# Kernel optimization log

Hardware: AMD Instinct MI355X
Metric: run time of the kernel (lower is better)

Reference implementation:

```python
import jax, jax.numpy as jnp
import numpy as np

E = 1024
H = 16
D = E // H  # head_dim = 64
B = 4
S = 2048


def setup_inputs() -> dict:
    key = jax.random.key(0)
    ks = jax.random.split(key, 10)
    sc = 1.0 / np.sqrt(E)
    return {
        "inputs": jax.random.normal(ks[0], (B, S, E), dtype=jnp.float32),
        "wq": jax.random.normal(ks[1], (E, E), dtype=jnp.float32) * sc,
        "bq": jnp.zeros((E,), dtype=jnp.float32),
        "wk": jax.random.normal(ks[2], (E, E), dtype=jnp.float32) * sc,
        "bk": jnp.zeros((E,), dtype=jnp.float32),
        "wv": jax.random.normal(ks[3], (E, E), dtype=jnp.float32) * sc,
        "bv": jnp.zeros((E,), dtype=jnp.float32),
        "wo": jax.random.normal(ks[4], (E, E), dtype=jnp.float32) * sc,
        "bo": jnp.zeros((E,), dtype=jnp.float32),
        "ln_gamma": jnp.ones((E,), dtype=jnp.float32),
        "ln_beta": jnp.zeros((E,), dtype=jnp.float32),
    }


def reference(inputs, wq, bq, wk, bk, wv, bv, wo, bo, ln_gamma, ln_beta):
    # QKV projections, split heads: [B,S,E] -> [B,H,S,D]
    def split_heads(x):
        return x.reshape(B, S, H, D).transpose(0, 2, 1, 3)

    q = split_heads(inputs @ wq + bq)
    k = split_heads(inputs @ wk + bk)
    v = split_heads(inputs @ wv + bv)

    scale = 1.0 / jnp.sqrt(jnp.asarray(D, dtype=inputs.dtype))
    score = jnp.einsum("bhqd,bhkd->bhqk", q, k) * scale  # [B,H,S,S]
    weights = jax.nn.softmax(score, axis=-1)
    out = jnp.einsum("bhqk,bhkd->bhqd", weights, v)  # [B,H,S,D]
    out = out.transpose(0, 2, 1, 3).reshape(B, S, E)
    out = out @ wo + bo

    # residual + LayerNorm(eps=1e-6)
    x = inputs + out
    mean = jnp.mean(x, axis=-1, keepdims=True)
    var = jnp.mean(jnp.square(x - mean), axis=-1, keepdims=True)
    x = (x - mean) * jax.lax.rsqrt(var + 1e-6)
    return x * ln_gamma + ln_beta
```

## Files before the change

### kernel.cpp

```cpp
#include <hip/hip_runtime.h>

#define E_DIM 1024
#define H_NUM 16
#define D_DIM 64
#define B_NUM 4
#define S_DIM 2048
#define M_DIM 8192

#define SCALE_Q 0.18033688011112042f
#define SMAX 10.0f

typedef _Float16 f16;
typedef __attribute__((ext_vector_type(4))) _Float16 f16x4;
typedef __attribute__((ext_vector_type(8))) _Float16 f16x8;
typedef __attribute__((ext_vector_type(2))) __fp16 h16x2;
typedef __attribute__((ext_vector_type(4))) float f32x4;

extern "C" __device__ float __ocml_native_exp2_f32(float);

#define MFMA32(a, b, c) __builtin_amdgcn_mfma_f32_16x16x32_f16(a, b, c, 0, 0, 0)

#define GLOBAL_LOAD_LDS_16(gp, lp)                                    \
  __builtin_amdgcn_global_load_lds(                                   \
      (const __attribute__((address_space(1))) void*)(gp),            \
      (__attribute__((address_space(3))) void*)(lp), 16, 0, 0)

__global__ __launch_bounds__(256) void k_convert_x(const float* __restrict__ x,
                                                   f16* __restrict__ xh) {
  size_t i = ((size_t)blockIdx.x * 256 + threadIdx.x) * 4;
  float4 v = *reinterpret_cast<const float4*>(x + i);
  f16x4 o = {(f16)v.x, (f16)v.y, (f16)v.z, (f16)v.w};
  *reinterpret_cast<f16x4*>(xh + i) = o;
}

__global__ __launch_bounds__(256) void k_transpose_w(
    const float* __restrict__ w0, const float* __restrict__ w1,
    const float* __restrict__ w2, const float* __restrict__ w3,
    f16* __restrict__ dst) {
  __shared__ float tile[32][33];
  const float* src = blockIdx.z == 0 ? w0 : blockIdx.z == 1 ? w1
                   : blockIdx.z == 2 ? w2 : w3;
  f16* out = dst + (size_t)blockIdx.z * (E_DIM * E_DIM);
  const int n0 = blockIdx.x * 32, k0 = blockIdx.y * 32;
  const int tx = threadIdx.x & 31, ty = threadIdx.x >> 5;
#pragma unroll
  for (int i = 0; i < 4; i++)
    tile[ty + i * 8][tx] = src[(size_t)(k0 + ty + i * 8) * E_DIM + n0 + tx];
  __syncthreads();
#pragma unroll
  for (int i = 0; i < 4; i++)
    out[(size_t)(n0 + ty + i * 8) * E_DIM + k0 + tx] = (f16)tile[tx][ty + i * 8];
}

__global__ __launch_bounds__(256) void k_gemm_qkv(
    const f16* __restrict__ A, const f16* __restrict__ BT3,
    const float* __restrict__ bq, const float* __restrict__ bk,
    const float* __restrict__ bv, f16* __restrict__ Qb,
    f16* __restrict__ Kb, f16* __restrict__ VT) {
  __shared__ short As[2][128 * 64];
  __shared__ short Bs[2][128 * 64];
  const int m0 = blockIdx.y * 128, n0 = blockIdx.x * 128;
  const int region = blockIdx.x >> 3;
  const float* bias = region == 0 ? bq : region == 1 ? bk : bv;
  const float scale = region == 0 ? SCALE_Q : 1.0f;
  const int t = threadIdx.x;
  const int wave = t >> 6, lane = t & 63;
  const int l15 = lane & 15, quad = lane >> 4;
  const int wm = (wave & 1) * 64, wn = (wave >> 1) * 64;
  const int er0 = t >> 3;
  const int ecs = (((t & 7) ^ (er0 & 7))) * 8;
  const int el = (t & 7) * 8;

  const f16* gA[4];
  const f16* gB[4];
  int eo[4];
#pragma unroll
  for (int i = 0; i < 4; i++) {
    const int r = er0 + i * 32;
    gA[i] = A + (size_t)(m0 + r) * E_DIM + ecs;
    gB[i] = BT3 + (size_t)(n0 + r) * E_DIM + ecs;
    eo[i] = r * 64 + el;
  }
  auto issue = [&](int bf) {
#pragma unroll
    for (int i = 0; i < 4; i++) {
      GLOBAL_LOAD_LDS_16(gA[i], &As[bf][eo[i]]);
      GLOBAL_LOAD_LDS_16(gB[i], &Bs[bf][eo[i]]);
      gA[i] += 64;
      gB[i] += 64;
    }
  };

  issue(0);
  f32x4 acc[4][4] = {};

  for (int kt = 0; kt < E_DIM / 64; kt++) {
    __syncthreads();
    if (kt + 1 < E_DIM / 64) issue((kt + 1) & 1);
    const short* as = As[kt & 1];
    const short* bs = Bs[kt & 1];
#pragma unroll
    for (int ks = 0; ks < 2; ks++) {
      f16x8 af[4], bfr[4];
#pragma unroll
      for (int i = 0; i < 4; i++) {
        const int cg = ((ks * 4 + quad) ^ (l15 & 7)) * 8;
        af[i]  = *reinterpret_cast<const f16x8*>(&as[(wm + i * 16 + l15) * 64 + cg]);
        bfr[i] = *reinterpret_cast<const f16x8*>(&bs[(wn + i * 16 + l15) * 64 + cg]);
      }
#pragma unroll
      for (int mi = 0; mi < 4; mi++)
#pragma unroll
        for (int ni = 0; ni < 4; ni++)
          acc[mi][ni] = MFMA32(af[mi], bfr[ni], acc[mi][ni]);
    }
  }
#pragma unroll
  for (int ni = 0; ni < 4; ni++) {
    const int col = ((n0 + wn + ni * 16 + l15) & 1023);
    const float bv_ = bias[col];
    const int hh = col >> 6, dd = col & 63;
#pragma unroll
    for (int mi = 0; mi < 4; mi++) {
#pragma unroll
      for (int r = 0; r < 4; r++) {
        const int row = m0 + wm + mi * 16 + quad * 4 + r;
        const f16 v = (f16)((acc[mi][ni][r] + bv_) * scale);
        if (region == 0) {
          Qb[(size_t)row * E_DIM + col] = v;
        } else if (region == 1) {
          Kb[(size_t)row * E_DIM + col] = v;
        } else {
          const int bb = row >> 11, ss = row & 2047;
          VT[(((size_t)bb * H_NUM + hh) * D_DIM + dd) * S_DIM + ss] = v;
        }
      }
    }
  }
}

__global__ __launch_bounds__(256) void k_gemm(
    const f16* __restrict__ A, const f16* __restrict__ BT,
    const float* __restrict__ bias, f16* __restrict__ Cout) {
  __shared__ short As[2][128 * 64];
  __shared__ short Bs[2][128 * 64];
  const int m0 = blockIdx.y * 128, n0 = blockIdx.x * 128;
  const int t = threadIdx.x;
  const int wave = t >> 6, lane = t & 63;
  const int l15 = lane & 15, quad = lane >> 4;
  const int wm = (wave & 1) * 64, wn = (wave >> 1) * 64;
  const int er0 = t >> 3;
  const int ecs = (((t & 7) ^ (er0 & 7))) * 8;
  const int el = (t & 7) * 8;

  const f16* gA[4];
  const f16* gB[4];
  int eo[4];
#pragma unroll
  for (int i = 0; i < 4; i++) {
    const int r = er0 + i * 32;
    gA[i] = A + (size_t)(m0 + r) * E_DIM + ecs;
    gB[i] = BT + (size_t)(n0 + r) * E_DIM + ecs;
    eo[i] = r * 64 + el;
  }
  auto issue = [&](int bf) {
#pragma unroll
    for (int i = 0; i < 4; i++) {
      GLOBAL_LOAD_LDS_16(gA[i], &As[bf][eo[i]]);
      GLOBAL_LOAD_LDS_16(gB[i], &Bs[bf][eo[i]]);
      gA[i] += 64;
      gB[i] += 64;
    }
  };

  issue(0);
  f32x4 acc[4][4] = {};

  for (int kt = 0; kt < E_DIM / 64; kt++) {
    __syncthreads();
    if (kt + 1 < E_DIM / 64) issue((kt + 1) & 1);
    const short* as = As[kt & 1];
    const short* bs = Bs[kt & 1];
#pragma unroll
    for (int ks = 0; ks < 2; ks++) {
      f16x8 af[4], bfr[4];
#pragma unroll
      for (int i = 0; i < 4; i++) {
        const int cg = ((ks * 4 + quad) ^ (l15 & 7)) * 8;
        af[i]  = *reinterpret_cast<const f16x8*>(&as[(wm + i * 16 + l15) * 64 + cg]);
        bfr[i] = *reinterpret_cast<const f16x8*>(&bs[(wn + i * 16 + l15) * 64 + cg]);
      }
#pragma unroll
      for (int mi = 0; mi < 4; mi++)
#pragma unroll
        for (int ni = 0; ni < 4; ni++)
          acc[mi][ni] = MFMA32(af[mi], bfr[ni], acc[mi][ni]);
    }
  }
#pragma unroll
  for (int ni = 0; ni < 4; ni++) {
    const int col = n0 + wn + ni * 16 + l15;
    const float bv = bias[col];
#pragma unroll
    for (int mi = 0; mi < 4; mi++) {
#pragma unroll
      for (int r = 0; r < 4; r++) {
        const int row = m0 + wm + mi * 16 + quad * 4 + r;
        Cout[(size_t)row * E_DIM + col] = (f16)(acc[mi][ni][r] + bv);
      }
    }
  }
}

__global__ __launch_bounds__(256) void k_attention(
    const f16* __restrict__ Q, const f16* __restrict__ K,
    const f16* __restrict__ VT, f16* __restrict__ O) {
  __shared__ short Ks[2][64 * 64];
  __shared__ short Vs[2][64 * 64];
  const int bh = blockIdx.x, qt = blockIdx.y;
  const int b = bh >> 4, h = bh & 15;
  const int t = threadIdx.x;
  const int wave = t >> 6, lane = t & 63, l15 = lane & 15, quad = lane >> 4;
  const size_t rowbase = (size_t)b * S_DIM;
  const int ch = h * D_DIM;
  const int qb = qt * 128 + wave * 32;

  f16x8 qf[2][2];
#pragma unroll
  for (int g = 0; g < 2; g++) {
    const size_t qrow = rowbase + qb + g * 16 + l15;
    qf[g][0] = *reinterpret_cast<const f16x8*>(Q + qrow * E_DIM + ch + quad * 8);
    qf[g][1] = *reinterpret_cast<const f16x8*>(Q + qrow * E_DIM + ch + 32 + quad * 8);
  }

  f32x4 o_acc[2][4] = {};
  f32x4 l_acc[2] = {};
  const f16x8 ones8 = {(f16)1.f, (f16)1.f, (f16)1.f, (f16)1.f,
                       (f16)1.f, (f16)1.f, (f16)1.f, (f16)1.f};

  const int cgp = lane & 7;
  const f16* vtb = VT + ((size_t)(b * H_NUM + h) * D_DIM) * S_DIM;
  const f16* kgp[2];
  const f16* vgp[2];
  int ofs[2];
#pragma unroll
  for (int i = 0; i < 2; i++) {
    const int slot = wave * 16 + i * 8 + (lane >> 3);
    const int nt = slot >> 4, qd = (slot >> 2) & 3, rr = slot & 3;
    const int p = (nt >> 1) * 32 + qd * 8 + (nt & 1) * 4 + rr;
    const int cgl = (cgp ^ (slot & 7)) * 8;
    kgp[i] = K + (rowbase + p) * E_DIM + ch + cgl;
    vgp[i] = vtb + (size_t)slot * S_DIM + cgl;
    ofs[i] = slot * 64 + cgp * 8;
  }

  auto issue = [&](int bf) {
#pragma unroll
    for (int i = 0; i < 2; i++) {
      GLOBAL_LOAD_LDS_16(kgp[i], &Ks[bf][ofs[i]]);
      GLOBAL_LOAD_LDS_16(vgp[i], &Vs[bf][ofs[i]]);
      kgp[i] += 64 * E_DIM;
      vgp[i] += 64;
    }
  };

  issue(0);

  for (int kt = 0; kt < S_DIM / 64; kt++) {
    __syncthreads();
    if (kt + 1 < S_DIM / 64) issue((kt + 1) & 1);
    const short* kb = &Ks[kt & 1][0];
    const short* vb = &Vs[kt & 1][0];

    f32x4 sacc[2][4];
#pragma unroll
    for (int g = 0; g < 2; g++)
#pragma unroll
      for (int nt = 0; nt < 4; nt++)
        sacc[g][nt] = (f32x4){-SMAX, -SMAX, -SMAX, -SMAX};
#pragma unroll
    for (int nt = 0; nt < 4; nt++) {
      f16x8 kf0 = *reinterpret_cast<const f16x8*>(
          &kb[(nt * 16 + l15) * 64 + (quad ^ (l15 & 7)) * 8]);
      f16x8 kf1 = *reinterpret_cast<const f16x8*>(
          &kb[(nt * 16 + l15) * 64 + ((4 | quad) ^ (l15 & 7)) * 8]);
#pragma unroll
      for (int g = 0; g < 2; g++) {
        sacc[g][nt] = MFMA32(kf0, qf[g][0], sacc[g][nt]);
        sacc[g][nt] = MFMA32(kf1, qf[g][1], sacc[g][nt]);
      }
    }

    f16x8 a8[2][2];
#pragma unroll
    for (int g = 0; g < 2; g++)
#pragma unroll
      for (int kk = 0; kk < 2; kk++) {
        union { f16x8 v8; h16x2 h2[4]; } u;
#pragma unroll
        for (int half = 0; half < 2; half++) {
          const f32x4 s4 = sacc[g][kk * 2 + half];
          u.h2[half * 2 + 0] = __builtin_amdgcn_cvt_pkrtz(
              __ocml_native_exp2_f32(s4[0]), __ocml_native_exp2_f32(s4[1]));
          u.h2[half * 2 + 1] = __builtin_amdgcn_cvt_pkrtz(
              __ocml_native_exp2_f32(s4[2]), __ocml_native_exp2_f32(s4[3]));
        }
        a8[g][kk] = u.v8;
      }

#pragma unroll
    for (int kk = 0; kk < 2; kk++) {
#pragma unroll
      for (int dt = 0; dt < 4; dt++) {
        f16x8 vf = *reinterpret_cast<const f16x8*>(
            &vb[(dt * 16 + l15) * 64 + ((kk * 4 + quad) ^ (l15 & 7)) * 8]);
#pragma unroll
        for (int g = 0; g < 2; g++)
          o_acc[g][dt] = MFMA32(a8[g][kk], vf, o_acc[g][dt]);
      }
#pragma unroll
      for (int g = 0; g < 2; g++)
        l_acc[g] = MFMA32(a8[g][kk], ones8, l_acc[g]);
    }
  }

#pragma unroll
  for (int g = 0; g < 2; g++) {
    const size_t obase = rowbase + qb + g * 16;
#pragma unroll
    for (int r = 0; r < 4; r++) {
      const float rl = 1.0f / l_acc[g][r];
#pragma unroll
      for (int dt = 0; dt < 4; dt++) {
        float v = o_acc[g][dt][r] * rl;
        O[(obase + quad * 4 + r) * E_DIM + ch + dt * 16 + l15] = (f16)v;
      }
    }
  }
}

__global__ __launch_bounds__(256) void k_ln(
    const f16* __restrict__ proj, const float* __restrict__ x,
    const float* __restrict__ gamma, const float* __restrict__ beta,
    float* __restrict__ out) {
  const int row = blockIdx.x;
  const int t = threadIdx.x;
  const size_t base = (size_t)row * E_DIM + t * 4;
  f16x4 p = *reinterpret_cast<const f16x4*>(proj + base);
  float4 xi = *reinterpret_cast<const float4*>(x + base);
  float v0 = (float)p[0] + xi.x, v1 = (float)p[1] + xi.y;
  float v2 = (float)p[2] + xi.z, v3 = (float)p[3] + xi.w;
  float s1 = v0 + v1 + v2 + v3;
  float s2 = v0 * v0 + v1 * v1 + v2 * v2 + v3 * v3;
#pragma unroll
  for (int off = 1; off < 64; off <<= 1) {
    s1 += __shfl_xor(s1, off, 64);
    s2 += __shfl_xor(s2, off, 64);
  }
  __shared__ float sh1[4], sh2[4];
  const int wave = t >> 6;
  if ((t & 63) == 0) { sh1[wave] = s1; sh2[wave] = s2; }
  __syncthreads();
  s1 = sh1[0] + sh1[1] + sh1[2] + sh1[3];
  s2 = sh2[0] + sh2[1] + sh2[2] + sh2[3];
  const float mean = s1 * (1.0f / E_DIM);
  const float var = s2 * (1.0f / E_DIM) - mean * mean;
  const float rstd = rsqrtf(var + 1e-6f);
  float4 g = *reinterpret_cast<const float4*>(gamma + t * 4);
  float4 bb = *reinterpret_cast<const float4*>(beta + t * 4);
  float4 o;
  o.x = (v0 - mean) * rstd * g.x + bb.x;
  o.y = (v1 - mean) * rstd * g.y + bb.y;
  o.z = (v2 - mean) * rstd * g.z + bb.z;
  o.w = (v3 - mean) * rstd * g.w + bb.w;
  *reinterpret_cast<float4*>(out + base) = o;
}

extern "C" void kernel_launch(void* const* d_in, const int* in_sizes, int n_in,
                              void* d_out, int out_size, void* d_ws, size_t ws_size,
                              hipStream_t stream) {
  const float* x     = (const float*)d_in[0];
  const float* wq    = (const float*)d_in[1];
  const float* bq    = (const float*)d_in[2];
  const float* wk    = (const float*)d_in[3];
  const float* bk    = (const float*)d_in[4];
  const float* wv    = (const float*)d_in[5];
  const float* bv    = (const float*)d_in[6];
  const float* wo    = (const float*)d_in[7];
  const float* bo    = (const float*)d_in[8];
  const float* gamma = (const float*)d_in[9];
  const float* beta  = (const float*)d_in[10];

  char* ws = (char*)d_ws;
  const size_t MB = 1ull << 20;
  f16* wt   = (f16*)(ws + 0 * MB);
  f16* wot  = (f16*)(ws + 6 * MB);
  f16* xh   = (f16*)(ws + 8 * MB);
  f16* Qb   = (f16*)(ws + 24 * MB);
  f16* Kb   = (f16*)(ws + 40 * MB);
  f16* VTb  = (f16*)(ws + 56 * MB);
  f16* Ob   = (f16*)(ws + 72 * MB);
  f16* proj = (f16*)(ws + 24 * MB);

  k_convert_x<<<M_DIM * E_DIM / 4 / 256, 256, 0, stream>>>(x, xh);
  k_transpose_w<<<dim3(32, 32, 4), 256, 0, stream>>>(wq, wk, wv, wo, wt);
  k_gemm_qkv<<<dim3(24, 64), 256, 0, stream>>>(xh, wt, bq, bk, bv, Qb, Kb, VTb);
  k_attention<<<dim3(B_NUM * H_NUM, S_DIM / 128), 256, 0, stream>>>(Qb, Kb, VTb, Ob);
  k_gemm<<<dim3(8, 64), 256, 0, stream>>>(Ob, wot, bo, proj);
  k_ln<<<M_DIM, 256, 0, stream>>>(proj, x, gamma, beta, (float*)d_out);
}
```

Measured before the change: 331.7 us.

## Use 256x128 GEMM tiles with triple-buffered LDS pipeline and block swizzle

Both projection GEMMs move from 128x128 tiles with 256 threads to 256x128 tiles with 512 threads. Global-to-LDS loads are now triple-buffered in dynamic shared memory, with explicit vmcnt waits so two tiles stay in flight. Block indices are remapped so neighbouring blocks share operand tiles in cache. The larger LDS footprint (144 KB) and higher register pressure may limit occupancy to one block per CU, and the grid shrinks to 768 and 256 blocks.

After: 315.6 us. 1.05x faster.

```diff
diff --git a/kernel.cpp b/kernel.cpp
--- a/kernel.cpp
+++ b/kernel.cpp
@@ -52,53 +52,77 @@
     out[(size_t)(n0 + ty + i * 8) * E_DIM + k0 + tx] = (f16)tile[tx][ty + i * 8];
 }
 
-__global__ __launch_bounds__(256) void k_gemm_qkv(
+
+__global__ __launch_bounds__(512) void k_gemm_qkv256(
     const f16* __restrict__ A, const f16* __restrict__ BT3,
     const float* __restrict__ bq, const float* __restrict__ bk,
     const float* __restrict__ bv, f16* __restrict__ Qb,
     f16* __restrict__ Kb, f16* __restrict__ VT) {
-  __shared__ short As[2][128 * 64];
-  __shared__ short Bs[2][128 * 64];
-  const int m0 = blockIdx.y * 128, n0 = blockIdx.x * 128;
-  const int region = blockIdx.x >> 3;
+  extern __shared__ short smem[];
+  short* Asb = smem;
+  short* Bsb = smem + 3 * 256 * 64;
+
+  const int w = (blockIdx.x & 7) * 96 + (blockIdx.x >> 3);
+  const int xt = w % 24, yt = w / 24;
+  const int m0 = yt * 256, n0 = xt * 128;
+  const int region = xt >> 3;
   const float* bias = region == 0 ? bq : region == 1 ? bk : bv;
   const float scale = region == 0 ? SCALE_Q : 1.0f;
+
   const int t = threadIdx.x;
   const int wave = t >> 6, lane = t & 63;
   const int l15 = lane & 15, quad = lane >> 4;
-  const int wm = (wave & 1) * 64, wn = (wave >> 1) * 64;
-  const int er0 = t >> 3;
-  const int ecs = (((t & 7) ^ (er0 & 7))) * 8;
-  const int el = (t & 7) * 8;
+  const int wm = (wave >> 1) * 64, wn = (wave & 1) * 64;
+
+  const int tr = t >> 3;
+  const int tc = t & 7;
+  const int swz = (tc ^ (tr & 7)) * 8;
+  const int el = tc * 8;
 
   const f16* gA[4];
-  const f16* gB[4];
-  int eo[4];
+  const f16* gB[2];
+  int eoA[4], eoB[2];
 #pragma unroll
   for (int i = 0; i < 4; i++) {
-    const int r = er0 + i * 32;
-    gA[i] = A + (size_t)(m0 + r) * E_DIM + ecs;
-    gB[i] = BT3 + (size_t)(n0 + r) * E_DIM + ecs;
-    eo[i] = r * 64 + el;
-  }
-  auto issue = [&](int bf) {
+    const int r = tr + i * 64;
+    gA[i] = A + (size_t)(m0 + r) * E_DIM + swz;
+    eoA[i] = r * 64 + el;
+  }
+#pragma unroll
+  for (int i = 0; i < 2; i++) {
+    const int r = tr + i * 64;
+    gB[i] = BT3 + (size_t)(n0 + r) * E_DIM + swz;
+    eoB[i] = r * 64 + el;
+  }
+  auto issue = [&](int b) {
+    short* ab = Asb + b * (256 * 64);
+    short* bb = Bsb + b * (128 * 64);
 #pragma unroll
     for (int i = 0; i < 4; i++) {
-      GLOBAL_LOAD_LDS_16(gA[i], &As[bf][eo[i]]);
-      GLOBAL_LOAD_LDS_16(gB[i], &Bs[bf][eo[i]]);
+      GLOBAL_LOAD_LDS_16(gA[i], ab + eoA[i]);
       gA[i] += 64;
+    }
+#pragma unroll
+    for (int i = 0; i < 2; i++) {
+      GLOBAL_LOAD_LDS_16(gB[i], bb + eoB[i]);
       gB[i] += 64;
     }
   };
 
   issue(0);
+  issue(1);
   f32x4 acc[4][4] = {};
 
+  int bsel = 0, bnext = 2;
   for (int kt = 0; kt < E_DIM / 64; kt++) {
-    __syncthreads();
-    if (kt + 1 < E_DIM / 64) issue((kt + 1) & 1);
-    const short* as = As[kt & 1];
-    const short* bs = Bs[kt & 1];
+    if (kt < E_DIM / 64 - 1)
+      asm volatile("s_waitcnt vmcnt(6)" ::: "memory");
+    else
+      asm volatile("s_waitcnt vmcnt(0)" ::: "memory");
+    __builtin_amdgcn_s_barrier();
+    if (kt < E_DIM / 64 - 2) issue(bnext);
+    const short* as = Asb + bsel * (256 * 64);
+    const short* bs = Bsb + bsel * (128 * 64);
 #pragma unroll
     for (int ks = 0; ks < 2; ks++) {
       f16x8 af[4], bfr[4];
@@ -114,10 +138,14 @@
         for (int ni = 0; ni < 4; ni++)
           acc[mi][ni] = MFMA32(af[mi], bfr[ni], acc[mi][ni]);
     }
-  }
+    asm volatile("s_waitcnt lgkmcnt(0)" ::: "memory");
+    bsel = bsel == 2 ? 0 : bsel + 1;
+    bnext = bnext == 2 ? 0 : bnext + 1;
+  }
+
 #pragma unroll
   for (int ni = 0; ni < 4; ni++) {
-    const int col = ((n0 + wn + ni * 16 + l15) & 1023);
+    const int col = (n0 + wn + ni * 16 + l15) & 1023;
     const float bv_ = bias[col];
     const int hh = col >> 6, dd = col & 63;
 #pragma unroll
@@ -139,48 +167,71 @@
   }
 }
 
-__global__ __launch_bounds__(256) void k_gemm(
+__global__ __launch_bounds__(512) void k_gemm_o256(
     const f16* __restrict__ A, const f16* __restrict__ BT,
     const float* __restrict__ bias, f16* __restrict__ Cout) {
-  __shared__ short As[2][128 * 64];
-  __shared__ short Bs[2][128 * 64];
-  const int m0 = blockIdx.y * 128, n0 = blockIdx.x * 128;
+  extern __shared__ short smem[];
+  short* Asb = smem;
+  short* Bsb = smem + 3 * 256 * 64;
+
+  const int w = (blockIdx.x & 7) * 32 + (blockIdx.x >> 3);
+  const int xt = w & 7, yt = w >> 3;
+  const int m0 = yt * 256, n0 = xt * 128;
+
   const int t = threadIdx.x;
   const int wave = t >> 6, lane = t & 63;
   const int l15 = lane & 15, quad = lane >> 4;
-  const int wm = (wave & 1) * 64, wn = (wave >> 1) * 64;
-  const int er0 = t >> 3;
-  const int ecs = (((t & 7) ^ (er0 & 7))) * 8;
-  const int el = (t & 7) * 8;
+  const int wm = (wave >> 1) * 64, wn = (wave & 1) * 64;
+
+  const int tr = t >> 3;
+  const int tc = t & 7;
+  const int swz = (tc ^ (tr & 7)) * 8;
+  const int el = tc * 8;
 
   const f16* gA[4];
-  const f16* gB[4];
-  int eo[4];
+  const f16* gB[2];
+  int eoA[4], eoB[2];
 #pragma unroll
   for (int i = 0; i < 4; i++) {
-    const int r = er0 + i * 32;
-    gA[i] = A + (size_t)(m0 + r) * E_DIM + ecs;
-    gB[i] = BT + (size_t)(n0 + r) * E_DIM + ecs;
-    eo[i] = r * 64 + el;
-  }
-  auto issue = [&](int bf) {
+    const int r = tr + i * 64;
+    gA[i] = A + (size_t)(m0 + r) * E_DIM + swz;
+    eoA[i] = r * 64 + el;
+  }
+#pragma unroll
+  for (int i = 0; i < 2; i++) {
+    const int r = tr + i * 64;
+    gB[i] = BT + (size_t)(n0 + r) * E_DIM + swz;
+    eoB[i] = r * 64 + el;
+  }
+  auto issue = [&](int b) {
+    short* ab = Asb + b * (256 * 64);
+    short* bb = Bsb + b * (128 * 64);
 #pragma unroll
     for (int i = 0; i < 4; i++) {
-      GLOBAL_LOAD_LDS_16(gA[i], &As[bf][eo[i]]);
-      GLOBAL_LOAD_LDS_16(gB[i], &Bs[bf][eo[i]]);
+      GLOBAL_LOAD_LDS_16(gA[i], ab + eoA[i]);
       gA[i] += 64;
+    }
+#pragma unroll
+    for (int i = 0; i < 2; i++) {
+      GLOBAL_LOAD_LDS_16(gB[i], bb + eoB[i]);
       gB[i] += 64;
     }
   };
 
   issue(0);
+  issue(1);
   f32x4 acc[4][4] = {};
 
+  int bsel = 0, bnext = 2;
   for (int kt = 0; kt < E_DIM / 64; kt++) {
-    __syncthreads();
-    if (kt + 1 < E_DIM / 64) issue((kt + 1) & 1);
-    const short* as = As[kt & 1];
-    const short* bs = Bs[kt & 1];
+    if (kt < E_DIM / 64 - 1)
+      asm volatile("s_waitcnt vmcnt(6)" ::: "memory");
+    else
+      asm volatile("s_waitcnt vmcnt(0)" ::: "memory");
+    __builtin_amdgcn_s_barrier();
+    if (kt < E_DIM / 64 - 2) issue(bnext);
+    const short* as = Asb + bsel * (256 * 64);
+    const short* bs = Bsb + bsel * (128 * 64);
 #pragma unroll
     for (int ks = 0; ks < 2; ks++) {
       f16x8 af[4], bfr[4];
@@ -196,7 +247,11 @@
         for (int ni = 0; ni < 4; ni++)
           acc[mi][ni] = MFMA32(af[mi], bfr[ni], acc[mi][ni]);
     }
-  }
+    asm volatile("s_waitcnt lgkmcnt(0)" ::: "memory");
+    bsel = bsel == 2 ? 0 : bsel + 1;
+    bnext = bnext == 2 ? 0 : bnext + 1;
+  }
+
 #pragma unroll
   for (int ni = 0; ni < 4; ni++) {
     const int col = n0 + wn + ni * 16 + l15;
@@ -402,10 +457,20 @@
   f16* Ob   = (f16*)(ws + 72 * MB);
   f16* proj = (f16*)(ws + 24 * MB);
 
+  const int GEMM_LDS = 3 * (256 * 64 + 128 * 64) * (int)sizeof(short);
+  static int attr_set = 0;
+  if (!attr_set) {
+    hipFuncSetAttribute((const void*)k_gemm_qkv256,
+                        hipFuncAttributeMaxDynamicSharedMemorySize, GEMM_LDS);
+    hipFuncSetAttribute((const void*)k_gemm_o256,
+                        hipFuncAttributeMaxDynamicSharedMemorySize, GEMM_LDS);
+    attr_set = 1;
+  }
+
   k_convert_x<<<M_DIM * E_DIM / 4 / 256, 256, 0, stream>>>(x, xh);
   k_transpose_w<<<dim3(32, 32, 4), 256, 0, stream>>>(wq, wk, wv, wo, wt);
-  k_gemm_qkv<<<dim3(24, 64), 256, 0, stream>>>(xh, wt, bq, bk, bv, Qb, Kb, VTb);
+  k_gemm_qkv256<<<768, 512, GEMM_LDS, stream>>>(xh, wt, bq, bk, bv, Qb, Kb, VTb);
   k_attention<<<dim3(B_NUM * H_NUM, S_DIM / 128), 256, 0, stream>>>(Qb, Kb, VTb, Ob);
-  k_gemm<<<dim3(8, 64), 256, 0, stream>>>(Ob, wot, bo, proj);
+  k_gemm_o256<<<256, 512, GEMM_LDS, stream>>>(Ob, wot, bo, proj);
   k_ln<<<M_DIM, 256, 0, stream>>>(proj, x, gamma, beta, (float*)d_out);
 }
```

## Rework GEMMs with 128x256 tiles, 3-stage LDS pipeline, XCD swizzle, MFMA priority

Applied to the files above, without the earlier changes.

Both projection GEMMs move to a shared mainloop using 512-thread blocks with 128x256 tiles, a triple-buffered LDS pipeline driven by explicit vmcnt waits, and a blockIdx remap that groups tiles per XCD for cache locality. MFMA sections get raised wave priority via s_setprio, and the attention kernel also gets setprio plus a launch-bounds occupancy hint and a constant-initialised score accumulator. The aim is to hide global-load latency and raise MFMA utilisation. The cost is about 144KB of dynamic LDS per block, which limits occupancy, and fragile hand-counted waitcnt values.

New measurement: 299.7 us. 1.11x faster.

```diff
diff --git a/kernel.cpp b/kernel.cpp
--- a/kernel.cpp
+++ b/kernel.cpp
@@ -52,80 +52,124 @@
     out[(size_t)(n0 + ty + i * 8) * E_DIM + k0 + tx] = (f16)tile[tx][ty + i * 8];
 }
 
-__global__ __launch_bounds__(256) void k_gemm_qkv(
+
+#define BK_T 64
+#define NKT (E_DIM / BK_T)
+#define SLOT_A (128 * BK_T)
+#define SLOT_B (256 * BK_T)
+#define GEMM_LDS_BYTES (3 * (SLOT_A + SLOT_B) * 2)
+
+__device__ __forceinline__ void gemm_mainloop_v3(
+    const f16* __restrict__ A, const f16* __restrict__ BT,
+    int m0, int n0, short* smem, f32x4 (&acc)[4][4]) {
+  short* Asb = smem;
+  short* Bsb = smem + 3 * SLOT_A;
+  const int t = threadIdx.x;
+  const int wave = t >> 6, lane = t & 63;
+  const int l15 = lane & 15, quad = lane >> 4;
+  const int wr = wave >> 2, wc = wave & 3;
+  const int tr = t >> 3, tc = t & 7;
+  const int swz = (tc ^ (tr & 7)) * 8;
+  const int el = tc * 8;
+
+  const f16* gA[2];
+  const f16* gB[4];
+  int eoA[2], eoB[4];
+#pragma unroll
+  for (int i = 0; i < 2; i++) {
+    gA[i] = A + (size_t)(m0 + i * 64 + tr) * E_DIM + swz;
+    eoA[i] = (i * 64 + tr) * 64 + el;
+  }
+#pragma unroll
+  for (int j = 0; j < 4; j++) {
+    gB[j] = BT + (size_t)(n0 + j * 64 + tr) * E_DIM + swz;
+    eoB[j] = (j * 64 + tr) * 64 + el;
+  }
+
+  auto stage = [&](int slot, int kt) {
+    short* ab = Asb + slot * SLOT_A;
+    short* bb = Bsb + slot * SLOT_B;
+    const int k0 = kt * BK_T;
+#pragma unroll
+    for (int i = 0; i < 2; i++) GLOBAL_LOAD_LDS_16(gA[i] + k0, ab + eoA[i]);
+#pragma unroll
+    for (int j = 0; j < 4; j++) GLOBAL_LOAD_LDS_16(gB[j] + k0, bb + eoB[j]);
+  };
+
+  stage(0, 0);
+  stage(1, 1);
+  stage(2, 2);
+
+  for (int kt = 0; kt < NKT; kt++) {
+    if (kt == 0)
+      asm volatile("s_waitcnt vmcnt(12)" ::: "memory");
+    else if (kt < NKT - 1)
+      asm volatile("s_waitcnt vmcnt(6)" ::: "memory");
+    else
+      asm volatile("s_waitcnt vmcnt(0)" ::: "memory");
+    __builtin_amdgcn_s_barrier();
+    if (kt >= 1 && kt + 2 < NKT) stage((kt + 2) % 3, kt + 2);
+
+    const short* as = Asb + (kt % 3) * SLOT_A;
+    const short* bs = Bsb + (kt % 3) * SLOT_B;
+    f16x8 af[4][2], bf[4][2];
+#pragma unroll
+    for (int mf = 0; mf < 4; mf++)
+#pragma unroll
+      for (int ks = 0; ks < 2; ks++)
+        af[mf][ks] = *reinterpret_cast<const f16x8*>(
+            &as[(wr * 64 + mf * 16 + l15) * 64 + ((ks * 4 + quad) ^ (l15 & 7)) * 8]);
+#pragma unroll
+    for (int nf = 0; nf < 4; nf++)
+#pragma unroll
+      for (int ks = 0; ks < 2; ks++)
+        bf[nf][ks] = *reinterpret_cast<const f16x8*>(
+            &bs[(wc * 64 + nf * 16 + l15) * 64 + ((ks * 4 + quad) ^ (l15 & 7)) * 8]);
+
+    __builtin_amdgcn_s_setprio(1);
+#pragma unroll
+    for (int mf = 0; mf < 4; mf++)
+#pragma unroll
+      for (int nf = 0; nf < 4; nf++) {
+        acc[mf][nf] = MFMA32(af[mf][0], bf[nf][0], acc[mf][nf]);
+        acc[mf][nf] = MFMA32(af[mf][1], bf[nf][1], acc[mf][nf]);
+      }
+    __builtin_amdgcn_s_setprio(0);
+    asm volatile("s_waitcnt lgkmcnt(0)" ::: "memory");
+  }
+}
+
+__global__ __launch_bounds__(512, 2) void k_gemm_qkv_v3(
     const f16* __restrict__ A, const f16* __restrict__ BT3,
     const float* __restrict__ bq, const float* __restrict__ bk,
     const float* __restrict__ bv, f16* __restrict__ Qb,
     f16* __restrict__ Kb, f16* __restrict__ VT) {
-  __shared__ short As[2][128 * 64];
-  __shared__ short Bs[2][128 * 64];
-  const int m0 = blockIdx.y * 128, n0 = blockIdx.x * 128;
-  const int region = blockIdx.x >> 3;
+  extern __shared__ short smem[];
+  const int w = (blockIdx.x & 7) * 96 + (blockIdx.x >> 3);
+  const int xt = w % 12, yt = w / 12;
+  const int m0 = yt * 128, n0 = xt * 256;
+  const int region = xt >> 2;
   const float* bias = region == 0 ? bq : region == 1 ? bk : bv;
   const float scale = region == 0 ? SCALE_Q : 1.0f;
+
+  f32x4 acc[4][4] = {};
+  gemm_mainloop_v3(A, BT3, m0, n0, smem, acc);
+
   const int t = threadIdx.x;
   const int wave = t >> 6, lane = t & 63;
   const int l15 = lane & 15, quad = lane >> 4;
-  const int wm = (wave & 1) * 64, wn = (wave >> 1) * 64;
-  const int er0 = t >> 3;
-  const int ecs = (((t & 7) ^ (er0 & 7))) * 8;
-  const int el = (t & 7) * 8;
-
-  const f16* gA[4];
-  const f16* gB[4];
-  int eo[4];
-#pragma unroll
-  for (int i = 0; i < 4; i++) {
-    const int r = er0 + i * 32;
-    gA[i] = A + (size_t)(m0 + r) * E_DIM + ecs;
-    gB[i] = BT3 + (size_t)(n0 + r) * E_DIM + ecs;
-    eo[i] = r * 64 + el;
-  }
-  auto issue = [&](int bf) {
-#pragma unroll
-    for (int i = 0; i < 4; i++) {
-      GLOBAL_LOAD_LDS_16(gA[i], &As[bf][eo[i]]);
-      GLOBAL_LOAD_LDS_16(gB[i], &Bs[bf][eo[i]]);
-      gA[i] += 64;
-      gB[i] += 64;
-    }
-  };
-
-  issue(0);
-  f32x4 acc[4][4] = {};
-
-  for (int kt = 0; kt < E_DIM / 64; kt++) {
-    __syncthreads();
-    if (kt + 1 < E_DIM / 64) issue((kt + 1) & 1);
-    const short* as = As[kt & 1];
-    const short* bs = Bs[kt & 1];
-#pragma unroll
-    for (int ks = 0; ks < 2; ks++) {
-      f16x8 af[4], bfr[4];
-#pragma unroll
-      for (int i = 0; i < 4; i++) {
-        const int cg = ((ks * 4 + quad) ^ (l15 & 7)) * 8;
-        af[i]  = *reinterpret_cast<const f16x8*>(&as[(wm + i * 16 + l15) * 64 + cg]);
-        bfr[i] = *reinterpret_cast<const f16x8*>(&bs[(wn + i * 16 + l15) * 64 + cg]);
-      }
-#pragma unroll
-      for (int mi = 0; mi < 4; mi++)
-#pragma unroll
-        for (int ni = 0; ni < 4; ni++)
-          acc[mi][ni] = MFMA32(af[mi], bfr[ni], acc[mi][ni]);
-    }
-  }
-#pragma unroll
-  for (int ni = 0; ni < 4; ni++) {
-    const int col = ((n0 + wn + ni * 16 + l15) & 1023);
+  const int wr = wave >> 2, wc = wave & 3;
+#pragma unroll
+  for (int nf = 0; nf < 4; nf++) {
+    const int col = (n0 + wc * 64 + nf * 16 + l15) & 1023;
     const float bv_ = bias[col];
     const int hh = col >> 6, dd = col & 63;
 #pragma unroll
-    for (int mi = 0; mi < 4; mi++) {
+    for (int mf = 0; mf < 4; mf++) {
 #pragma unroll
       for (int r = 0; r < 4; r++) {
-        const int row = m0 + wm + mi * 16 + quad * 4 + r;
-        const f16 v = (f16)((acc[mi][ni][r] + bv_) * scale);
+        const int row = m0 + wr * 64 + mf * 16 + quad * 4 + r;
+        const f16 v = (f16)((acc[mf][nf][r] + bv_) * scale);
         if (region == 0) {
           Qb[(size_t)row * E_DIM + col] = v;
         } else if (region == 1) {
@@ -139,80 +183,37 @@
   }
 }
 
-__global__ __launch_bounds__(256) void k_gemm(
+__global__ __launch_bounds__(512, 2) void k_gemm_o_v3(
     const f16* __restrict__ A, const f16* __restrict__ BT,
     const float* __restrict__ bias, f16* __restrict__ Cout) {
-  __shared__ short As[2][128 * 64];
-  __shared__ short Bs[2][128 * 64];
-  const int m0 = blockIdx.y * 128, n0 = blockIdx.x * 128;
+  extern __shared__ short smem[];
+  const int w = (blockIdx.x & 7) * 32 + (blockIdx.x >> 3);
+  const int xt = w & 3, yt = w >> 2;
+  const int m0 = yt * 128, n0 = xt * 256;
+
+  f32x4 acc[4][4] = {};
+  gemm_mainloop_v3(A, BT, m0, n0, smem, acc);
+
   const int t = threadIdx.x;
   const int wave = t >> 6, lane = t & 63;
   const int l15 = lane & 15, quad = lane >> 4;
-  const int wm = (wave & 1) * 64, wn = (wave >> 1) * 64;
-  const int er0 = t >> 3;
-  const int ecs = (((t & 7) ^ (er0 & 7))) * 8;
-  const int el = (t & 7) * 8;
-
-  const f16* gA[4];
-  const f16* gB[4];
-  int eo[4];
-#pragma unroll
-  for (int i = 0; i < 4; i++) {
-    const int r = er0 + i * 32;
-    gA[i] = A + (size_t)(m0 + r) * E_DIM + ecs;
-    gB[i] = BT + (size_t)(n0 + r) * E_DIM + ecs;
-    eo[i] = r * 64 + el;
-  }
-  auto issue = [&](int bf) {
-#pragma unroll
-    for (int i = 0; i < 4; i++) {
-      GLOBAL_LOAD_LDS_16(gA[i], &As[bf][eo[i]]);
-      GLOBAL_LOAD_LDS_16(gB[i], &Bs[bf][eo[i]]);
-      gA[i] += 64;
-      gB[i] += 64;
-    }
-  };
-
-  issue(0);
-  f32x4 acc[4][4] = {};
-
-  for (int kt = 0; kt < E_DIM / 64; kt++) {
-    __syncthreads();
-    if (kt + 1 < E_DIM / 64) issue((kt + 1) & 1);
-    const short* as = As[kt & 1];
-    const short* bs = Bs[kt & 1];
-#pragma unroll
-    for (int ks = 0; ks < 2; ks++) {
-      f16x8 af[4], bfr[4];
-#pragma unroll
-      for (int i = 0; i < 4; i++) {
-        const int cg = ((ks * 4 + quad) ^ (l15 & 7)) * 8;
-        af[i]  = *reinterpret_cast<const f16x8*>(&as[(wm + i * 16 + l15) * 64 + cg]);
-        bfr[i] = *reinterpret_cast<const f16x8*>(&bs[(wn + i * 16 + l15) * 64 + cg]);
-      }
-#pragma unroll
-      for (int mi = 0; mi < 4; mi++)
-#pragma unroll
-        for (int ni = 0; ni < 4; ni++)
-          acc[mi][ni] = MFMA32(af[mi], bfr[ni], acc[mi][ni]);
-    }
-  }
-#pragma unroll
-  for (int ni = 0; ni < 4; ni++) {
-    const int col = n0 + wn + ni * 16 + l15;
+  const int wr = wave >> 2, wc = wave & 3;
+#pragma unroll
+  for (int nf = 0; nf < 4; nf++) {
+    const int col = n0 + wc * 64 + nf * 16 + l15;
     const float bv = bias[col];
 #pragma unroll
-    for (int mi = 0; mi < 4; mi++) {
+    for (int mf = 0; mf < 4; mf++) {
 #pragma unroll
       for (int r = 0; r < 4; r++) {
-        const int row = m0 + wm + mi * 16 + quad * 4 + r;
-        Cout[(size_t)row * E_DIM + col] = (f16)(acc[mi][ni][r] + bv);
-      }
-    }
-  }
-}
-
-__global__ __launch_bounds__(256) void k_attention(
+        const int row = m0 + wr * 64 + mf * 16 + quad * 4 + r;
+        Cout[(size_t)row * E_DIM + col] = (f16)(acc[mf][nf][r] + bv);
+      }
+    }
+  }
+}
+
+__global__ __launch_bounds__(256, 4) void k_attention(
     const f16* __restrict__ Q, const f16* __restrict__ K,
     const f16* __restrict__ VT, f16* __restrict__ O) {
   __shared__ short Ks[2][64 * 64];
@@ -237,6 +238,7 @@
   f32x4 l_acc[2] = {};
   const f16x8 ones8 = {(f16)1.f, (f16)1.f, (f16)1.f, (f16)1.f,
                        (f16)1.f, (f16)1.f, (f16)1.f, (f16)1.f};
+  const f32x4 cinit = {-SMAX, -SMAX, -SMAX, -SMAX};
 
   const int cgp = lane & 7;
   const f16* vtb = VT + ((size_t)(b * H_NUM + h) * D_DIM) * S_DIM;
@@ -273,11 +275,7 @@
     const short* vb = &Vs[kt & 1][0];
 
     f32x4 sacc[2][4];
-#pragma unroll
-    for (int g = 0; g < 2; g++)
-#pragma unroll
-      for (int nt = 0; nt < 4; nt++)
-        sacc[g][nt] = (f32x4){-SMAX, -SMAX, -SMAX, -SMAX};
+    __builtin_amdgcn_s_setprio(1);
 #pragma unroll
     for (int nt = 0; nt < 4; nt++) {
       f16x8 kf0 = *reinterpret_cast<const f16x8*>(
@@ -286,10 +284,11 @@
           &kb[(nt * 16 + l15) * 64 + ((4 | quad) ^ (l15 & 7)) * 8]);
 #pragma unroll
       for (int g = 0; g < 2; g++) {
-        sacc[g][nt] = MFMA32(kf0, qf[g][0], sacc[g][nt]);
+        sacc[g][nt] = MFMA32(kf0, qf[g][0], cinit);
         sacc[g][nt] = MFMA32(kf1, qf[g][1], sacc[g][nt]);
       }
     }
+    __builtin_amdgcn_s_setprio(0);
 
     f16x8 a8[2][2];
 #pragma unroll
@@ -308,6 +307,7 @@
         a8[g][kk] = u.v8;
       }
 
+    __builtin_amdgcn_s_setprio(1);
 #pragma unroll
     for (int kk = 0; kk < 2; kk++) {
 #pragma unroll
@@ -322,6 +322,7 @@
       for (int g = 0; g < 2; g++)
         l_acc[g] = MFMA32(a8[g][kk], ones8, l_acc[g]);
     }
+    __builtin_amdgcn_s_setprio(0);
   }
 
 #pragma unroll
@@ -402,10 +403,19 @@
   f16* Ob   = (f16*)(ws + 72 * MB);
   f16* proj = (f16*)(ws + 24 * MB);
 
+  static int attr_set = 0;
+  if (!attr_set) {
+    hipFuncSetAttribute((const void*)k_gemm_qkv_v3,
+                        hipFuncAttributeMaxDynamicSharedMemorySize, GEMM_LDS_BYTES);
+    hipFuncSetAttribute((const void*)k_gemm_o_v3,
+                        hipFuncAttributeMaxDynamicSharedMemorySize, GEMM_LDS_BYTES);
+    attr_set = 1;
+  }
+
   k_convert_x<<<M_DIM * E_DIM / 4 / 256, 256, 0, stream>>>(x, xh);
   k_transpose_w<<<dim3(32, 32, 4), 256, 0, stream>>>(wq, wk, wv, wo, wt);
-  k_gemm_qkv<<<dim3(24, 64), 256, 0, stream>>>(xh, wt, bq, bk, bv, Qb, Kb, VTb);
+  k_gemm_qkv_v3<<<768, 512, GEMM_LDS_BYTES, stream>>>(xh, wt, bq, bk, bv, Qb, Kb, VTb);
   k_attention<<<dim3(B_NUM * H_NUM, S_DIM / 128), 256, 0, stream>>>(Qb, Kb, VTb, Ob);
-  k_gemm<<<dim3(8, 64), 256, 0, stream>>>(Ob, wot, bo, proj);
+  k_gemm_o_v3<<<256, 512, GEMM_LDS_BYTES, stream>>>(Ob, wot, bo, proj);
   k_ln<<<M_DIM, 256, 0, stream>>>(proj, x, gamma, beta, (float*)d_out);
 }
```
